# Optimization experiments

Measured on AMD Instinct MI355X. Metric: run time of the kernel, lower is better.

## Reference

```python
import jax, jax.numpy as jnp
import numpy as np

N, E = 50000, 800000
F_IN, HID, HEADS, OUT = 128, 32, 4, 16
NEG_SLOPE = 0.2  # PyG GATConv default leaky_relu slope


def segment_softmax(logits, seg, n):
    # numerically stable softmax over edges grouped by destination node
    m = jax.ops.segment_max(logits, seg, num_segments=n)          # [N,H]
    m = jnp.where(jnp.isfinite(m), m, 0.0)                        # guard empty segments
    e = jnp.exp(logits - m[seg])                                  # [E,H]
    s = jax.ops.segment_sum(e, seg, num_segments=n)               # [N,H]
    return e / (s[seg] + 1e-16)


def gat_conv(x, W, a_src, a_dst, bias, src, dst, concat):
    H, C = a_src.shape
    n = x.shape[0]
    h = (x @ W).reshape(n, H, C)                                  # [N,H,C]
    alpha_src = jnp.einsum('nhc,hc->nh', h, a_src)                # [N,H]
    alpha_dst = jnp.einsum('nhc,hc->nh', h, a_dst)                # [N,H]
    e = jax.nn.leaky_relu(alpha_src[src] + alpha_dst[dst], NEG_SLOPE)  # [E,H]
    alpha = segment_softmax(e, dst, n)                            # [E,H]
    msg = h[src] * alpha[:, :, None]                              # [E,H,C]
    out = jax.ops.segment_sum(msg, dst, num_segments=n)           # [N,H,C]
    out = out.reshape(n, H * C) if concat else out.mean(axis=1)
    return out + bias


def setup_inputs() -> dict:
    key = jax.random.key(0)
    ks = jax.random.split(key, 12)
    s = 0.1  # keep attention logits in a sane range
    return {
        'x': jax.random.normal(ks[0], (N, F_IN), jnp.float32),
        'edge_index': jax.random.randint(ks[1], (2, E), 0, N),
        'Wemb': jax.random.normal(ks[2], (F_IN, HID), jnp.float32) * s,
        'bemb': jnp.zeros((HID,), jnp.float32),
        'W1': jax.random.normal(ks[3], (HID, HEADS * HID), jnp.float32) * s,
        'a_src1': jax.random.normal(ks[4], (HEADS, HID), jnp.float32) * s,
        'a_dst1': jax.random.normal(ks[5], (HEADS, HID), jnp.float32) * s,
        'b1': jnp.zeros((HEADS * HID,), jnp.float32),
        'W2': jax.random.normal(ks[6], (HEADS * HID, HEADS * OUT), jnp.float32) * s,
        'a_src2': jax.random.normal(ks[7], (HEADS, OUT), jnp.float32) * s,
        'a_dst2': jax.random.normal(ks[8], (HEADS, OUT), jnp.float32) * s,
        'b2': jnp.zeros((OUT,), jnp.float32),
    }


def reference(x, edge_index, Wemb, bemb, W1, a_src1, a_dst1, b1, W2, a_src2, a_dst2, b2):
    src, dst = edge_index[0], edge_index[1]
    h = x @ Wemb + bemb  # dropout layers are identity at inference
    h = jax.nn.elu(gat_conv(h, W1, a_src1, a_dst1, b1, src, dst, True))
    h = gat_conv(h, W2, a_src2, a_dst2, b2, src, dst, False)
    return jax.nn.log_softmax(h, axis=1)
```

## Files before the change

### kernel.cpp

```cpp
#include <hip/hip_runtime.h>

#define N_NODES 50000
#define N_EDGES 800000
#define F_IN    128
#define HID     32
#define HEADS   4
#define OUT_C   16

#define NBKT 196
#define CAP  5120
#define EPB  4096
#define NB64 782

typedef __attribute__((ext_vector_type(8))) short bf16x8;
typedef __attribute__((ext_vector_type(4))) float f32x4;

__device__ __forceinline__ unsigned short f2bf(float f) {
    unsigned int u = __float_as_uint(f);
    u += 0x7FFFu + ((u >> 16) & 1u);
    return (unsigned short)(u >> 16);
}
__device__ __forceinline__ float bf_lo(unsigned int u) { return __uint_as_float(u << 16); }
__device__ __forceinline__ float bf_hi(unsigned int u) { return __uint_as_float(u & 0xFFFF0000u); }
__device__ __forceinline__ float bf2f(unsigned short s) {
    return __uint_as_float(((unsigned int)s) << 16);
}

__device__ __forceinline__ float edge_w(float asv, float adv) {
    float v = asv + adv;
    v = (v > 0.f) ? v : 0.2f * v;
    return __expf(v);
}

__global__ __launch_bounds__(256) void k_F1(const float* __restrict__ x,
                                            const float* __restrict__ Wemb,
                                            const float* __restrict__ bemb,
                                            float* __restrict__ h0,
                                            unsigned short* __restrict__ h0b,
                                            const int* __restrict__ ei,
                                            int* __restrict__ gcnt,
                                            unsigned int* __restrict__ pairs) {
    __shared__ float xs[64][132];
    __shared__ float Wl[F_IN][HID];
    __shared__ float bl[HID];
    __shared__ int hist[NBKT];
    __shared__ int base[NBKT];
    int t = threadIdx.x;
    if (blockIdx.x < NB64) {
        int node0 = blockIdx.x * 64;
        if (t < HID) bl[t] = bemb[t];
        #pragma unroll
        for (int it = 0; it < 4; it++) {
            int idx = it * 256 + t;
            *(float4*)((float*)Wl + idx * 4) = *(const float4*)(Wemb + idx * 4);
        }
        #pragma unroll
        for (int it = 0; it < 8; it++) {
            int idx = it * 256 + t;
            int row = idx >> 5, c4 = idx & 31;
            float4 v = make_float4(0.f, 0.f, 0.f, 0.f);
            if (node0 + row < N_NODES) v = *(const float4*)(x + (size_t)(node0 + row) * F_IN + c4 * 4);
            *(float4*)&xs[row][c4 * 4] = v;
        }
        __syncthreads();
        int c = t & 7, g = t >> 3;
        float acc[2][4] = {};
        for (int k = 0; k < F_IN; k++) {
            float4 w4 = *(const float4*)&Wl[k][c * 4];
            #pragma unroll
            for (int n = 0; n < 2; n++) {
                float xv = xs[g * 2 + n][k];
                acc[n][0] += xv * w4.x; acc[n][1] += xv * w4.y;
                acc[n][2] += xv * w4.z; acc[n][3] += xv * w4.w;
            }
        }
        #pragma unroll
        for (int n = 0; n < 2; n++) {
            int node = node0 + g * 2 + n;
            if (node < N_NODES) {
                float4 o = make_float4(acc[n][0] + bl[c * 4], acc[n][1] + bl[c * 4 + 1],
                                       acc[n][2] + bl[c * 4 + 2], acc[n][3] + bl[c * 4 + 3]);
                *(float4*)(h0 + (size_t)node * HID + c * 4) = o;
                ushort4 ob;
                ob.x = f2bf(o.x); ob.y = f2bf(o.y); ob.z = f2bf(o.z); ob.w = f2bf(o.w);
                *(ushort4*)(h0b + (size_t)node * HID + c * 4) = ob;
            }
        }
    } else {
        int e0 = (blockIdx.x - NB64) * EPB;
        for (int i = t; i < NBKT; i += 256) hist[i] = 0;
        __syncthreads();
        unsigned int p[16];
        int bb[16];
        #pragma unroll
        for (int i = 0; i < 16; i++) {
            int e = e0 + i * 256 + t;
            bb[i] = -1;
            if (e < N_EDGES) {
                int s = ei[e], d = ei[N_EDGES + e];
                p[i] = ((unsigned int)s << 8) | (unsigned int)(d & 255);
                bb[i] = d >> 8;
                atomicAdd(&hist[bb[i]], 1);
            }
        }
        __syncthreads();
        for (int i = t; i < NBKT; i += 256) {
            int c = hist[i];
            base[i] = i * CAP + (c ? atomicAdd(&gcnt[i], c) : 0);
            hist[i] = 0;
        }
        __syncthreads();
        #pragma unroll
        for (int i = 0; i < 16; i++) {
            if (bb[i] >= 0) {
                int off = atomicAdd(&hist[bb[i]], 1);
                pairs[base[bb[i]] + off] = p[i];
            }
        }
    }
}

__global__ __launch_bounds__(256) void k_F2(const float* __restrict__ h0,
                                            const float* __restrict__ W1,
                                            const float* __restrict__ a_src,
                                            const float* __restrict__ a_dst,
                                            float* __restrict__ as, float* __restrict__ ad,
                                            const unsigned int* __restrict__ pairs,
                                            const int* __restrict__ gcnt,
                                            int* __restrict__ rowptr,
                                            int* __restrict__ esrc) {
    __shared__ float xs[64][36];
    __shared__ float Wl[HID][128];
    __shared__ int cnt[256];
    __shared__ int cur[256];
    __shared__ int wsum[4];
    int t = threadIdx.x;
    if (blockIdx.x < NB64) {
        int node0 = blockIdx.x * 64;
        #pragma unroll
        for (int it = 0; it < 4; it++) {
            int idx = it * 256 + t;
            *(float4*)((float*)Wl + idx * 4) = *(const float4*)(W1 + idx * 4);
        }
        #pragma unroll
        for (int it = 0; it < 2; it++) {
            int idx = it * 256 + t;
            int row = idx >> 3, c4 = idx & 7;
            float4 v = make_float4(0.f, 0.f, 0.f, 0.f);
            if (node0 + row < N_NODES) v = *(const float4*)(h0 + (size_t)(node0 + row) * HID + c4 * 4);
            *(float4*)&xs[row][c4 * 4] = v;
        }
        __syncthreads();
        int c = t & 31, g = t >> 5;
        float acc[8][4] = {};
        for (int k = 0; k < HID; k++) {
            float4 w4 = *(const float4*)&Wl[k][c * 4];
            #pragma unroll
            for (int n = 0; n < 8; n++) {
                float xv = xs[g * 8 + n][k];
                acc[n][0] += xv * w4.x; acc[n][1] += xv * w4.y;
                acc[n][2] += xv * w4.z; acc[n][3] += xv * w4.w;
            }
        }
        float4 av = *(const float4*)(a_src + c * 4);
        float4 dv = *(const float4*)(a_dst + c * 4);
        float ps[8], pd[8];
        #pragma unroll
        for (int n = 0; n < 8; n++) {
            ps[n] = acc[n][0] * av.x + acc[n][1] * av.y + acc[n][2] * av.z + acc[n][3] * av.w;
            pd[n] = acc[n][0] * dv.x + acc[n][1] * dv.y + acc[n][2] * dv.z + acc[n][3] * dv.w;
        }
        #pragma unroll
        for (int mask = 1; mask <= 4; mask <<= 1) {
            #pragma unroll
            for (int n = 0; n < 8; n++) {
                ps[n] += __shfl_xor(ps[n], mask, 64);
                pd[n] += __shfl_xor(pd[n], mask, 64);
            }
        }
        if ((c & 7) == 0) {
            int hh = c >> 3;
            #pragma unroll
            for (int n = 0; n < 8; n++) {
                int node = node0 + g * 8 + n;
                if (node < N_NODES) { as[node * 4 + hh] = ps[n]; ad[node * 4 + hh] = pd[n]; }
            }
        }
    } else {
        int b = blockIdx.x - NB64;
        int lane = t & 63, wv = t >> 6;
        int v0 = (t < NBKT && t < b) ? gcnt[t] : 0;
        #pragma unroll
        for (int mask = 1; mask < 64; mask <<= 1) v0 += __shfl_xor(v0, mask, 64);
        if (lane == 0) wsum[wv] = v0;
        __syncthreads();
        int base = wsum[0] + wsum[1] + wsum[2] + wsum[3];
        int n0 = b << 8;
        int cntb = gcnt[b];
        int s0 = b * CAP;
        cnt[t] = 0;
        __syncthreads();
        for (int i = t; i < cntb; i += 256) atomicAdd(&cnt[pairs[s0 + i] & 255], 1);
        __syncthreads();
        int v = cnt[t], x = v;
        #pragma unroll
        for (int off = 1; off < 64; off <<= 1) { int y = __shfl_up(x, off, 64); if (lane >= off) x += y; }
        __syncthreads();
        if (lane == 63) wsum[wv] = x;
        __syncthreads();
        int add = 0;
        for (int j = 0; j < wv; j++) add += wsum[j];
        int excl = base + (x - v) + add;
        cur[t] = excl;
        if (n0 + t < N_NODES) rowptr[n0 + t] = excl;
        if (b == 0 && t == 0) rowptr[N_NODES] = N_EDGES;
        __syncthreads();
        for (int i = t; i < cntb; i += 256) {
            unsigned int p = pairs[s0 + i];
            int pos = atomicAdd(&cur[p & 255], 1);
            esrc[pos] = (int)(p >> 8);
        }
    }
}

__global__ __launch_bounds__(256) void k_gather1(const int* __restrict__ esrc,
                                                 const int* __restrict__ rowptr,
                                                 const unsigned int* __restrict__ h0b,
                                                 const float* __restrict__ as,
                                                 const float* __restrict__ ad,
                                                 unsigned int* __restrict__ awb) {
    int t = threadIdx.x;
    int node = blockIdx.x * 4 + (t >> 6);
    int lane = t & 63;
    int head = lane >> 4;
    int cp = lane & 15;
    int s16 = lane >> 2;
    int h4 = lane & 3;
    int lb = cp * 4;
    int hb = head * 4;
    int beg = rowptr[node], end = rowptr[node + 1];
    float ad_w = ad[node * 4 + h4];
    float ax = 0.f, ay = 0.f, s = 0.f;
    const char* hc = (const char*)h0b;
    for (int k = beg; k < end; k += 16) {
        int idx = k + s16;
        int sm = esrc[min(idx, end - 1)];
#define G1L(J) int sj##J = __builtin_amdgcn_readlane(sm, (J) * 4); \
        unsigned int u##J = *(const unsigned int*)(hc + (size_t)(unsigned)sj##J * 64 + lb);
        G1L(0)  G1L(1)  G1L(2)  G1L(3)  G1L(4)  G1L(5)  G1L(6)  G1L(7)
        G1L(8)  G1L(9)  G1L(10) G1L(11) G1L(12) G1L(13) G1L(14) G1L(15)
#undef G1L
        float wm = edge_w(as[sm * 4 + h4], ad_w);
        if (idx >= end) wm = 0.f;
        int wmi = __float_as_int(wm);
#define G1W(J) float w##J = __int_as_float(__builtin_amdgcn_ds_bpermute(hb + (J) * 16, wmi));
        G1W(0)  G1W(1)  G1W(2)  G1W(3)  G1W(4)  G1W(5)  G1W(6)  G1W(7)
        G1W(8)  G1W(9)  G1W(10) G1W(11) G1W(12) G1W(13) G1W(14) G1W(15)
#undef G1W
        ax += bf_lo(u0)  * w0  + bf_lo(u1)  * w1  + bf_lo(u2)  * w2  + bf_lo(u3)  * w3
            + bf_lo(u4)  * w4  + bf_lo(u5)  * w5  + bf_lo(u6)  * w6  + bf_lo(u7)  * w7
            + bf_lo(u8)  * w8  + bf_lo(u9)  * w9  + bf_lo(u10) * w10 + bf_lo(u11) * w11
            + bf_lo(u12) * w12 + bf_lo(u13) * w13 + bf_lo(u14) * w14 + bf_lo(u15) * w15;
        ay += bf_hi(u0)  * w0  + bf_hi(u1)  * w1  + bf_hi(u2)  * w2  + bf_hi(u3)  * w3
            + bf_hi(u4)  * w4  + bf_hi(u5)  * w5  + bf_hi(u6)  * w6  + bf_hi(u7)  * w7
            + bf_hi(u8)  * w8  + bf_hi(u9)  * w9  + bf_hi(u10) * w10 + bf_hi(u11) * w11
            + bf_hi(u12) * w12 + bf_hi(u13) * w13 + bf_hi(u14) * w14 + bf_hi(u15) * w15;
        s += (w0 + w1 + w2 + w3) + (w4 + w5 + w6 + w7)
           + (w8 + w9 + w10 + w11) + (w12 + w13 + w14 + w15);
    }
    float rs = 1.0f / (s + 1e-16f);
    awb[(size_t)node * 64 + lane] = ((unsigned int)f2bf(ay * rs) << 16) | (unsigned int)f2bf(ax * rs);
}

__global__ __launch_bounds__(256) void k_h12(const unsigned int* __restrict__ awb,
                                             const float* __restrict__ W1,
                                             const float* __restrict__ b1,
                                             const float* __restrict__ W2,
                                             const float* __restrict__ a_src,
                                             const float* __restrict__ a_dst,
                                             unsigned short* __restrict__ h2,
                                             float* __restrict__ as, float* __restrict__ ad) {
    __shared__ unsigned int xsu[64][68];
    __shared__ unsigned short w1t[128][40];
    __shared__ unsigned short w2t[64][136];
    __shared__ float b1s[128];
    int t = threadIdx.x;
    int node0 = blockIdx.x * 64;
    if (t < 128) b1s[t] = b1[t];
    #pragma unroll
    for (int it = 0; it < 4; it++) {
        int idx = it * 256 + t;
        int row = idx >> 4, c4 = idx & 15;
        uint4 v = make_uint4(0u, 0u, 0u, 0u);
        if (node0 + row < N_NODES) v = *(const uint4*)(awb + (size_t)(node0 + row) * 64 + c4 * 4);
        *(uint4*)&xsu[row][c4 * 4] = v;
    }
    #pragma unroll
    for (int it = 0; it < 16; it++) {
        int idx = it * 256 + t;
        int k = idx >> 7, n = idx & 127;
        w1t[n][k] = f2bf(W1[idx]);
    }
    #pragma unroll
    for (int it = 0; it < 8; it++) {
        int idx = it * 256 + t;
        int k = idx >> 4, n4 = idx & 15;
        float4 w = *(const float4*)(W2 + k * 64 + n4 * 4);
        w2t[n4 * 4 + 0][k] = f2bf(w.x);
        w2t[n4 * 4 + 1][k] = f2bf(w.y);
        w2t[n4 * 4 + 2][k] = f2bf(w.z);
        w2t[n4 * 4 + 3][k] = f2bf(w.w);
    }
    __syncthreads();
    int lane = t & 63, wv = t >> 6;
    int lrow = lane & 15, lk = lane >> 4;
    const char* abase = (const char*)&xsu[wv * 16 + lrow][0];
    f32x4 o1[8];
    #pragma unroll
    for (int nt = 0; nt < 8; nt++) {
        int kt = nt >> 1;
        bf16x8 af = *(const bf16x8*)(abase + kt * 64 + lk * 16);
        bf16x8 bf1 = *(const bf16x8*)((const char*)&w1t[nt * 16 + lrow][0] + lk * 16);
        f32x4 z = {};
        o1[nt] = __builtin_amdgcn_mfma_f32_16x16x32_bf16(af, bf1, z, 0, 0, 0);
    }
    __syncthreads();
    unsigned short* o1t = (unsigned short*)&xsu[0][0];
    #pragma unroll
    for (int nt = 0; nt < 8; nt++) {
        float bb = b1s[nt * 16 + lrow];
        #pragma unroll
        for (int r = 0; r < 4; r++) {
            int noderow = wv * 16 + lk * 4 + r;
            float v = o1[nt][r] + bb;
            v = (v > 0.f) ? v : (__expf(v) - 1.0f);
            o1t[noderow * 136 + nt * 16 + lrow] = f2bf(v);
        }
    }
    __syncthreads();
    f32x4 acc[4] = {};
    const char* xbase = (const char*)&o1t[(wv * 16 + lrow) * 136];
    #pragma unroll
    for (int kt = 0; kt < 4; kt++) {
        bf16x8 af = *(const bf16x8*)(xbase + kt * 64 + lk * 16);
        #pragma unroll
        for (int h = 0; h < 4; h++) {
            bf16x8 bfr = *(const bf16x8*)((const char*)&w2t[h * 16 + lrow][0] + kt * 64 + lk * 16);
            acc[h] = __builtin_amdgcn_mfma_f32_16x16x32_bf16(af, bfr, acc[h], 0, 0, 0);
        }
    }
    float av[4], dv[4];
    #pragma unroll
    for (int h = 0; h < 4; h++) { av[h] = a_src[h * 16 + lrow]; dv[h] = a_dst[h * 16 + lrow]; }
    #pragma unroll
    for (int r = 0; r < 4; r++) {
        int node = node0 + wv * 16 + lk * 4 + r;
        float psh[4], pdh[4];
        #pragma unroll
        for (int h = 0; h < 4; h++) {
            float v = acc[h][r];
            if (node < N_NODES) h2[(size_t)node * 64 + h * 16 + lrow] = f2bf(v);
            float p = v * av[h], q = v * dv[h];
            #pragma unroll
            for (int mask = 1; mask < 16; mask <<= 1) {
                p += __shfl_xor(p, mask, 64);
                q += __shfl_xor(q, mask, 64);
            }
            psh[h] = p; pdh[h] = q;
        }
        if (lrow == 0 && node < N_NODES) {
            *(float4*)(as + node * 4) = make_float4(psh[0], psh[1], psh[2], psh[3]);
            *(float4*)(ad + node * 4) = make_float4(pdh[0], pdh[1], pdh[2], pdh[3]);
        }
    }
}

__global__ __launch_bounds__(256) void k_gather2(const int* __restrict__ esrc,
                                                 const int* __restrict__ rowptr,
                                                 const unsigned short* __restrict__ h2,
                                                 const float* __restrict__ as,
                                                 const float* __restrict__ ad,
                                                 const float* __restrict__ b2,
                                                 float* __restrict__ out) {
    int t = threadIdx.x;
    int node = blockIdx.x * 4 + (t >> 6);
    int lane = t & 63;
    int head = lane >> 4, c = lane & 15;
    int s16 = lane >> 2;
    int h4 = lane & 3;
    int lb = lane * 2;
    int hb = head * 4;
    int beg = rowptr[node], end = rowptr[node + 1];
    float ad_w = ad[node * 4 + h4];
    float acc = 0.f, s = 0.f;
    const char* h2c = (const char*)h2;
    for (int k = beg; k < end; k += 16) {
        int idx = k + s16;
        int sm = esrc[min(idx, end - 1)];
#define G2L(J) int sj##J = __builtin_amdgcn_readlane(sm, (J) * 4); \
        float r##J = bf2f(*(const unsigned short*)(h2c + (size_t)(unsigned)sj##J * 128 + lb));
        G2L(0)  G2L(1)  G2L(2)  G2L(3)  G2L(4)  G2L(5)  G2L(6)  G2L(7)
        G2L(8)  G2L(9)  G2L(10) G2L(11) G2L(12) G2L(13) G2L(14) G2L(15)
#undef G2L
        float wm = edge_w(as[sm * 4 + h4], ad_w);
        if (idx >= end) wm = 0.f;
        int wmi = __float_as_int(wm);
#define G2W(J) float w##J = __int_as_float(__builtin_amdgcn_ds_bpermute(hb + (J) * 16, wmi));
        G2W(0)  G2W(1)  G2W(2)  G2W(3)  G2W(4)  G2W(5)  G2W(6)  G2W(7)
        G2W(8)  G2W(9)  G2W(10) G2W(11) G2W(12) G2W(13) G2W(14) G2W(15)
#undef G2W
        acc += r0 * w0 + r1 * w1 + r2 * w2 + r3 * w3
             + r4 * w4 + r5 * w5 + r6 * w6 + r7 * w7
             + r8 * w8 + r9 * w9 + r10 * w10 + r11 * w11
             + r12 * w12 + r13 * w13 + r14 * w14 + r15 * w15;
        s += (w0 + w1 + w2 + w3) + (w4 + w5 + w6 + w7)
           + (w8 + w9 + w10 + w11) + (w12 + w13 + w14 + w15);
    }
    float v = acc * (1.0f / (s + 1e-16f));
    v += __shfl_xor(v, 16, 64);
    v += __shfl_xor(v, 32, 64);
    v = v * 0.25f + b2[c];
    float m = v;
    #pragma unroll
    for (int mask = 1; mask < 16; mask <<= 1) m = fmaxf(m, __shfl_xor(m, mask, 64));
    float ex = __expf(v - m);
    float se = ex;
    #pragma unroll
    for (int mask = 1; mask < 16; mask <<= 1) se += __shfl_xor(se, mask, 64);
    float res = (v - m) - __logf(se);
    if (lane < 16) out[(size_t)node * 16 + lane] = res;
}

extern "C" void kernel_launch(void* const* d_in, const int* in_sizes, int n_in,
                              void* d_out, int out_size, void* d_ws, size_t ws_size,
                              hipStream_t stream) {
    const float* x      = (const float*)d_in[0];
    const int*   ei     = (const int*)d_in[1];
    const float* Wemb   = (const float*)d_in[2];
    const float* bemb   = (const float*)d_in[3];
    const float* W1     = (const float*)d_in[4];
    const float* a_src1 = (const float*)d_in[5];
    const float* a_dst1 = (const float*)d_in[6];
    const float* b1     = (const float*)d_in[7];
    const float* W2     = (const float*)d_in[8];
    const float* a_src2 = (const float*)d_in[9];
    const float* a_dst2 = (const float*)d_in[10];
    const float* b2     = (const float*)d_in[11];
    float* out = (float*)d_out;

    char* ws = (char*)d_ws;
    size_t off = 0;
    auto alloc = [&](size_t bytes) { char* p = ws + off; off += (bytes + 255) & ~size_t(255); return p; };
    unsigned short* h2b   = (unsigned short*)alloc((size_t)N_NODES * 64 * 2);
    unsigned int*   awb   = (unsigned int*)alloc((size_t)N_NODES * 64 * 4);
    float*        h0    = (float*)alloc((size_t)N_NODES * HID * 4);
    unsigned short* h0b = (unsigned short*)alloc((size_t)N_NODES * HID * 2);
    int*          esrc  = (int*)alloc((size_t)N_EDGES * 4 + 64);
    unsigned int* pairs = (unsigned int*)alloc((size_t)NBKT * CAP * 4);
    float* as     = (float*)alloc((size_t)N_NODES * 4 * 4);
    float* ad     = (float*)alloc((size_t)N_NODES * 4 * 4);
    int*   rowptr = (int*)alloc((size_t)(N_NODES + 1) * 4);
    int*   gcnt   = (int*)alloc((size_t)NBKT * 4);

    const int GB = N_NODES / 4;

    hipMemsetAsync(gcnt, 0, (size_t)NBKT * 4, stream);
    k_F1<<<NB64 + NBKT, 256, 0, stream>>>(x, Wemb, bemb, h0, h0b, ei, gcnt, pairs);
    k_F2<<<NB64 + NBKT, 256, 0, stream>>>(h0, W1, a_src1, a_dst1, as, ad,
                                          pairs, gcnt, rowptr, esrc);
    k_gather1<<<GB, 256, 0, stream>>>(esrc, rowptr, (const unsigned int*)h0b, as, ad, awb);
    k_h12<<<NB64, 256, 0, stream>>>(awb, W1, b1, W2, a_src2, a_dst2, h2b, as, ad);
    k_gather2<<<GB, 256, 0, stream>>>(esrc, rowptr, h2b, as, ad, b2, out);
}
```

Measured before the change: 192.3 us.

## Fold W1·a projections into embedding kernel and drop h0 fp32 buffer

Precomputes the vectors W1·a_src and W1·a_dst per block so the layer-1 attention logits come straight from the embedding output inside k_F1. This removes the separate 32x128 GEMM pass in k_F2 and the fp32 h0 write and reread, which leaves k_F2 doing only CSR construction over the buckets. Each embedding block now recomputes a small 32x4x2 weight-vector product and adds shuffle reductions. It also changes the floating-point summation order of the logits.

New measurement: 192.8 us. About the same (+0.2%).

```diff
diff --git a/kernel.cpp b/kernel.cpp
--- a/kernel.cpp
+++ b/kernel.cpp
@@ -35,20 +35,34 @@
 __global__ __launch_bounds__(256) void k_F1(const float* __restrict__ x,
                                             const float* __restrict__ Wemb,
                                             const float* __restrict__ bemb,
-                                            float* __restrict__ h0,
+                                            const float* __restrict__ W1,
+                                            const float* __restrict__ a_src,
+                                            const float* __restrict__ a_dst,
                                             unsigned short* __restrict__ h0b,
+                                            float* __restrict__ as, float* __restrict__ ad,
                                             const int* __restrict__ ei,
                                             int* __restrict__ gcnt,
                                             unsigned int* __restrict__ pairs) {
     __shared__ float xs[64][132];
     __shared__ float Wl[F_IN][HID];
     __shared__ float bl[HID];
+    __shared__ float vs[HID][4];
+    __shared__ float vd[HID][4];
     __shared__ int hist[NBKT];
     __shared__ int base[NBKT];
     int t = threadIdx.x;
     if (blockIdx.x < NB64) {
         int node0 = blockIdx.x * 64;
         if (t < HID) bl[t] = bemb[t];
+        {
+            int k = (t & 127) >> 2, h = t & 3;
+            const float* wrow = W1 + k * 128 + h * 32;
+            const float* arow = ((t < 128) ? a_src : a_dst) + h * 32;
+            float accv = 0.f;
+            #pragma unroll
+            for (int c2 = 0; c2 < 32; c2++) accv += wrow[c2] * arow[c2];
+            if (t < 128) vs[k][h] = accv; else vd[k][h] = accv;
+        }
         #pragma unroll
         for (int it = 0; it < 4; it++) {
             int idx = it * 256 + t;
@@ -74,16 +88,46 @@
                 acc[n][2] += xv * w4.z; acc[n][3] += xv * w4.w;
             }
         }
+        float ps[2][4], pd[2][4];
         #pragma unroll
         for (int n = 0; n < 2; n++) {
+            float o0 = acc[n][0] + bl[c * 4];
+            float o1 = acc[n][1] + bl[c * 4 + 1];
+            float o2 = acc[n][2] + bl[c * 4 + 2];
+            float o3 = acc[n][3] + bl[c * 4 + 3];
             int node = node0 + g * 2 + n;
             if (node < N_NODES) {
-                float4 o = make_float4(acc[n][0] + bl[c * 4], acc[n][1] + bl[c * 4 + 1],
-                                       acc[n][2] + bl[c * 4 + 2], acc[n][3] + bl[c * 4 + 3]);
-                *(float4*)(h0 + (size_t)node * HID + c * 4) = o;
                 ushort4 ob;
-                ob.x = f2bf(o.x); ob.y = f2bf(o.y); ob.z = f2bf(o.z); ob.w = f2bf(o.w);
+                ob.x = f2bf(o0); ob.y = f2bf(o1); ob.z = f2bf(o2); ob.w = f2bf(o3);
                 *(ushort4*)(h0b + (size_t)node * HID + c * 4) = ob;
+            }
+            #pragma unroll
+            for (int h = 0; h < 4; h++) {
+                ps[n][h] = o0 * vs[c * 4][h] + o1 * vs[c * 4 + 1][h]
+                         + o2 * vs[c * 4 + 2][h] + o3 * vs[c * 4 + 3][h];
+                pd[n][h] = o0 * vd[c * 4][h] + o1 * vd[c * 4 + 1][h]
+                         + o2 * vd[c * 4 + 2][h] + o3 * vd[c * 4 + 3][h];
+            }
+        }
+        #pragma unroll
+        for (int mask = 1; mask <= 4; mask <<= 1) {
+            #pragma unroll
+            for (int n = 0; n < 2; n++) {
+                #pragma unroll
+                for (int h = 0; h < 4; h++) {
+                    ps[n][h] += __shfl_xor(ps[n][h], mask, 64);
+                    pd[n][h] += __shfl_xor(pd[n][h], mask, 64);
+                }
+            }
+        }
+        if (c == 0) {
+            #pragma unroll
+            for (int n = 0; n < 2; n++) {
+                int node = node0 + g * 2 + n;
+                if (node < N_NODES) {
+                    *(float4*)(as + node * 4) = make_float4(ps[n][0], ps[n][1], ps[n][2], ps[n][3]);
+                    *(float4*)(ad + node * 4) = make_float4(pd[n][0], pd[n][1], pd[n][2], pd[n][3]);
+                }
             }
         }
     } else {
@@ -120,106 +164,46 @@
     }
 }
 
-__global__ __launch_bounds__(256) void k_F2(const float* __restrict__ h0,
-                                            const float* __restrict__ W1,
-                                            const float* __restrict__ a_src,
-                                            const float* __restrict__ a_dst,
-                                            float* __restrict__ as, float* __restrict__ ad,
-                                            const unsigned int* __restrict__ pairs,
+__global__ __launch_bounds__(256) void k_F2(const unsigned int* __restrict__ pairs,
                                             const int* __restrict__ gcnt,
                                             int* __restrict__ rowptr,
                                             int* __restrict__ esrc) {
-    __shared__ float xs[64][36];
-    __shared__ float Wl[HID][128];
     __shared__ int cnt[256];
     __shared__ int cur[256];
     __shared__ int wsum[4];
     int t = threadIdx.x;
-    if (blockIdx.x < NB64) {
-        int node0 = blockIdx.x * 64;
-        #pragma unroll
-        for (int it = 0; it < 4; it++) {
-            int idx = it * 256 + t;
-            *(float4*)((float*)Wl + idx * 4) = *(const float4*)(W1 + idx * 4);
-        }
-        #pragma unroll
-        for (int it = 0; it < 2; it++) {
-            int idx = it * 256 + t;
-            int row = idx >> 3, c4 = idx & 7;
-            float4 v = make_float4(0.f, 0.f, 0.f, 0.f);
-            if (node0 + row < N_NODES) v = *(const float4*)(h0 + (size_t)(node0 + row) * HID + c4 * 4);
-            *(float4*)&xs[row][c4 * 4] = v;
-        }
-        __syncthreads();
-        int c = t & 31, g = t >> 5;
-        float acc[8][4] = {};
-        for (int k = 0; k < HID; k++) {
-            float4 w4 = *(const float4*)&Wl[k][c * 4];
-            #pragma unroll
-            for (int n = 0; n < 8; n++) {
-                float xv = xs[g * 8 + n][k];
-                acc[n][0] += xv * w4.x; acc[n][1] += xv * w4.y;
-                acc[n][2] += xv * w4.z; acc[n][3] += xv * w4.w;
-            }
-        }
-        float4 av = *(const float4*)(a_src + c * 4);
-        float4 dv = *(const float4*)(a_dst + c * 4);
-        float ps[8], pd[8];
-        #pragma unroll
-        for (int n = 0; n < 8; n++) {
-            ps[n] = acc[n][0] * av.x + acc[n][1] * av.y + acc[n][2] * av.z + acc[n][3] * av.w;
-            pd[n] = acc[n][0] * dv.x + acc[n][1] * dv.y + acc[n][2] * dv.z + acc[n][3] * dv.w;
-        }
-        #pragma unroll
-        for (int mask = 1; mask <= 4; mask <<= 1) {
-            #pragma unroll
-            for (int n = 0; n < 8; n++) {
-                ps[n] += __shfl_xor(ps[n], mask, 64);
-                pd[n] += __shfl_xor(pd[n], mask, 64);
-            }
-        }
-        if ((c & 7) == 0) {
-            int hh = c >> 3;
-            #pragma unroll
-            for (int n = 0; n < 8; n++) {
-                int node = node0 + g * 8 + n;
-                if (node < N_NODES) { as[node * 4 + hh] = ps[n]; ad[node * 4 + hh] = pd[n]; }
-            }
-        }
-    } else {
-        int b = blockIdx.x - NB64;
-        int lane = t & 63, wv = t >> 6;
-        int v0 = (t < NBKT && t < b) ? gcnt[t] : 0;
-        #pragma unroll
-        for (int mask = 1; mask < 64; mask <<= 1) v0 += __shfl_xor(v0, mask, 64);
-        if (lane == 0) wsum[wv] = v0;
-        __syncthreads();
-        int base = wsum[0] + wsum[1] + wsum[2] + wsum[3];
-        int n0 = b << 8;
-        int cntb = gcnt[b];
-        int s0 = b * CAP;
-        cnt[t] = 0;
-        __syncthreads();
-        for (int i = t; i < cntb; i += 256) atomicAdd(&cnt[pairs[s0 + i] & 255], 1);
-        __syncthreads();
-        int v = cnt[t], x = v;
-        #pragma unroll
-        for (int off = 1; off < 64; off <<= 1) { int y = __shfl_up(x, off, 64); if (lane >= off) x += y; }
-        __syncthreads();
-        if (lane == 63) wsum[wv] = x;
-        __syncthreads();
-        int add = 0;
-        for (int j = 0; j < wv; j++) add += wsum[j];
-        int excl = base + (x - v) + add;
-        cur[t] = excl;
-        if (n0 + t < N_NODES) rowptr[n0 + t] = excl;
-        if (b == 0 && t == 0) rowptr[N_NODES] = N_EDGES;
-        __syncthreads();
-        for (int i = t; i < cntb; i += 256) {
-            unsigned int p = pairs[s0 + i];
-            int pos = atomicAdd(&cur[p & 255], 1);
-            esrc[pos] = (int)(p >> 8);
-        }
+    int b = blockIdx.x;
+    int lane = t & 63, wv = t >> 6;
+    int v0 = (t < NBKT && t < b) ? gcnt[t] : 0;
+    #pragma unroll
+    for (int mask = 1; mask < 64; mask <<= 1) v0 += __shfl_xor(v0, mask, 64);
+    if (lane == 0) wsum[wv] = v0;
+    __syncthreads();
+    int base = wsum[0] + wsum[1] + wsum[2] + wsum[3];
+    int n0 = b << 8;
+    int cntb = gcnt[b];
+    int s0 = b * CAP;
+    cnt[t] = 0;
+    __syncthreads();
+    for (int i = t; i < cntb; i += 256) atomicAdd(&cnt[pairs[s0 + i] & 255], 1);
+    __syncthreads();
+    int v = cnt[t], x = v;
+    #pragma unroll
+    for (int off = 1; off < 64; off <<= 1) { int y = __shfl_up(x, off, 64); if (lane >= off) x += y; }
+    __syncthreads();
+    if (lane == 63) wsum[wv] = x;
+    __syncthreads();
+    int add = 0;
+    for (int j = 0; j < wv; j++) add += wsum[j];
+    int excl = base + (x - v) + add;
+    cur[t] = excl;
+    if (n0 + t < N_NODES) rowptr[n0 + t] = excl;
+    if (b == 0 && t == 0) rowptr[N_NODES] = N_EDGES;
+    __syncthreads();
+    for (int i = t; i < cntb; i += 256) {
+        unsigned int p = pairs[s0 + i];
+        int pos = atomicAdd(&cur[p & 255], 1);
+        esrc[pos] = (int)(p >> 8);
     }
 }
 
@@ -453,7 +437,6 @@
     auto alloc = [&](size_t bytes) { char* p = ws + off; off += (bytes + 255) & ~size_t(255); return p; };
     unsigned short* h2b   = (unsigned short*)alloc((size_t)N_NODES * 64 * 2);
     unsigned int*   awb   = (unsigned int*)alloc((size_t)N_NODES * 64 * 4);
-    float*        h0    = (float*)alloc((size_t)N_NODES * HID * 4);
     unsigned short* h0b = (unsigned short*)alloc((size_t)N_NODES * HID * 2);
     int*          esrc  = (int*)alloc((size_t)N_EDGES * 4 + 64);
     unsigned int* pairs = (unsigned int*)alloc((size_t)NBKT * CAP * 4);
@@ -465,9 +448,9 @@
     const int GB = N_NODES / 4;
 
     hipMemsetAsync(gcnt, 0, (size_t)NBKT * 4, stream);
-    k_F1<<<NB64 + NBKT, 256, 0, stream>>>(x, Wemb, bemb, h0, h0b, ei, gcnt, pairs);
-    k_F2<<<NB64 + NBKT, 256, 0, stream>>>(h0, W1, a_src1, a_dst1, as, ad,
-                                          pairs, gcnt, rowptr, esrc);
+    k_F1<<<NB64 + NBKT, 256, 0, stream>>>(x, Wemb, bemb, W1, a_src1, a_dst1,
+                                          h0b, as, ad, ei, gcnt, pairs);
+    k_F2<<<NBKT, 256, 0, stream>>>(pairs, gcnt, rowptr, esrc);
     k_gather1<<<GB, 256, 0, stream>>>(esrc, rowptr, (const unsigned int*)h0b, as, ad, awb);
     k_h12<<<NB64, 256, 0, stream>>>(awb, W1, b1, W2, a_src2, a_dst2, h2b, as, ad);
     k_gather2<<<GB, 256, 0, stream>>>(esrc, rowptr, h2b, as, ad, b2, out);
```
